# Optimization experiments

Measured on AMD Instinct MI355X. Metric: run time of the kernel, lower is better.

## Reference

```python
import jax, jax.numpy as jnp
import numpy as np

HIDDEN = 128
NUM_TYPES = 13
LN_EPS = 1e-5


def setup_inputs() -> dict:
    key = jax.random.key(0)
    k_adj, k_emb, k_idx, k_w, k_b = jax.random.split(key, 5)
    B, N, M, H, T = 8, 4096, 2048, HIDDEN, NUM_TYPES
    adj = jax.random.uniform(k_adj, (B, N, M), dtype=jnp.float32)
    embeds = jax.random.normal(k_emb, (B, N, H), dtype=jnp.float32)
    node_type_index = jax.random.randint(k_idx, (B, N), 0, T, dtype=jnp.int32)
    node_mask = jnp.ones((B, N), dtype=bool)
    # per-type Linear params (nn.Linear default init ~ U(-1/sqrt(H), 1/sqrt(H)))
    lim = 1.0 / np.sqrt(H)
    W = jax.random.uniform(k_w, (T, H, H), dtype=jnp.float32, minval=-lim, maxval=lim)
    b = jax.random.uniform(k_b, (T, H), dtype=jnp.float32, minval=-lim, maxval=lim)
    gamma = jnp.ones((H,), dtype=jnp.float32)
    beta = jnp.zeros((H,), dtype=jnp.float32)
    return {"adj": adj, "embeds": embeds, "node_type_index": node_type_index,
            "node_mask": node_mask, "W": W, "b": b, "gamma": gamma, "beta": beta}


def reference(adj, embeds, node_type_index, node_mask, W, b, gamma, beta):
    T = W.shape[0]
    # per-node-type linear: compute all T projections, then route by type.
    # y: [T, B, N, H]
    y = jnp.einsum('bnh,thd->tbnd', embeds, W) + b[:, None, None, :]
    onehot = jax.nn.one_hot(node_type_index, T, dtype=embeds.dtype)  # [B, N, T]
    routed = jnp.einsum('tbnd,bnt->bnd', y, onehot)                   # [B, N, H]
    x = jnp.where(node_mask[..., None], routed, embeds)
    # LayerNorm over hidden dim
    mu = jnp.mean(x, axis=-1, keepdims=True)
    var = jnp.mean(jnp.square(x - mu), axis=-1, keepdims=True)
    x = (x - mu) * jax.lax.rsqrt(var + LN_EPS) * gamma + beta
    # two-stage hypergraph aggregation: adj^T @ x, then adj @ lat
    lat = jnp.einsum('bnm,bnh->bmh', adj, x)   # [B, M, H]
    ret = jnp.einsum('bnm,bmh->bnh', adj, lat)  # [B, N, H]
    return ret
```

## Files before the change

### kernel.cpp

```cpp
#include <hip/hip_runtime.h>
#include <stdint.h>
#include <stddef.h>


typedef float    f32x4_t  __attribute__((ext_vector_type(4)));
typedef __bf16   bf16x8_t __attribute__((ext_vector_type(8)));
typedef unsigned int u32x4_t __attribute__((ext_vector_type(4)));
typedef unsigned int u32x2_t __attribute__((ext_vector_type(2)));

__device__ __forceinline__ unsigned short f2bf(float f) {
    union { float f; unsigned int u; } v; v.f = f;
    unsigned int u = v.u;
    return (unsigned short)((u + 0x7FFFu + ((u >> 16) & 1u)) >> 16);
}

__device__ __forceinline__ unsigned int cvtpk(float a, float b) {
    unsigned int r;
    asm("v_cvt_pk_bf16_f32 %0, %1, %2" : "=v"(r) : "v"(a), "v"(b));
    return r;
}

__device__ __forceinline__ bool mask_on(const unsigned char* m, int gid) {
    return (m[gid] | m[(gid >> 2) << 2]) != 0;
}

__device__ __forceinline__ int foff(int row, int g) {
    return row * 128 + (((g) ^ (row & 7)) << 4);
}

template<int GSTRIDE>
__device__ __forceinline__ void stage_B(const unsigned short* __restrict__ gb,
                                        int k0, unsigned short* ldsB, int t)
{
    const int l = t & 63, w = t >> 6;
    const int hsub = l >> 3;
    const int csrc = ((l & 7) ^ hsub) << 3;
    #pragma unroll
    for (int i = 0; i < 4; ++i) {
        const int hbase = i * 32 + w * 8;
        const unsigned short* src = gb + (size_t)(hbase + hsub) * GSTRIDE + k0 + csrc;
        unsigned short* dst = ldsB + hbase * 64;
        __builtin_amdgcn_global_load_lds(
            (__attribute__((address_space(1))) void*)src,
            (__attribute__((address_space(3))) void*)dst, 16, 0, 0);
    }
}

__global__ __launch_bounds__(256) void k0_wtrans(
    const float* __restrict__ W, unsigned short* __restrict__ WT)
{
    __shared__ float tile[128][132];
    const int t = threadIdx.x, ty = blockIdx.x;
    const float* Wt = W + (size_t)ty * 128 * 128;
    for (int it = 0; it < 16; ++it) {
        int idx = it * 256 + t;
        int h = idx >> 5, c = (idx & 31) * 4;
        *(float4*)(&tile[h][c]) = *(const float4*)(Wt + h * 128 + c);
    }
    __syncthreads();
    const int d = t >> 1, half = t & 1, h0 = half * 64;
    unsigned short* out = WT + ((size_t)ty * 128 + d) * 128 + h0;
    #pragma unroll
    for (int ch = 0; ch < 8; ++ch) {
        int h = h0 + ch * 8;
        u32x4_t o;
        o[0] = cvtpk(tile[h + 0][d], tile[h + 1][d]);
        o[1] = cvtpk(tile[h + 2][d], tile[h + 3][d]);
        o[2] = cvtpk(tile[h + 4][d], tile[h + 5][d]);
        o[3] = cvtpk(tile[h + 6][d], tile[h + 7][d]);
        *(u32x4_t*)(out + ch * 8) = o;
    }
}

__global__ __launch_bounds__(256) void k1_typed_ln(
    const float* __restrict__ embeds,
    const int*   __restrict__ ntype,
    const unsigned char* __restrict__ mask8,
    const unsigned short* __restrict__ WT,
    const float* __restrict__ bias,
    const float* __restrict__ gamma,
    const float* __restrict__ beta,
    unsigned short* __restrict__ xT)
{
    __shared__ unsigned short e_lds[64][136];
    __shared__ unsigned short y_lds[64][136];
    __shared__ unsigned short lists[13][64];
    __shared__ int cnt[13];
    __shared__ int grp_ty[32], grp_base[32], grp_n;
    __shared__ unsigned char msk[64];
    __shared__ float g_lds[128], be_lds[128];

    const int t   = threadIdx.x;
    const int bid = blockIdx.x;
    const int b   = bid & 7;
    const int n0  = (bid >> 3) << 6;
    const int gbase = b * 4096 + n0;
    const float* ebase = embeds + (size_t)gbase * 128;

    {
        const int n = t >> 2, q = t & 3;
        const float* src = ebase + n * 128 + q * 32;
        #pragma unroll
        for (int c = 0; c < 4; ++c) {
            f32x4_t va = *(const f32x4_t*)(src + c * 8);
            f32x4_t vb = *(const f32x4_t*)(src + c * 8 + 4);
            u32x4_t o;
            o[0] = cvtpk(va[0], va[1]); o[1] = cvtpk(va[2], va[3]);
            o[2] = cvtpk(vb[0], vb[1]); o[3] = cvtpk(vb[2], vb[3]);
            *(u32x4_t*)(&e_lds[n][q * 32 + c * 8]) = o;
        }
    }
    if (t < 128) { g_lds[t] = gamma[t]; be_lds[t] = beta[t]; }
    if (t < 64)  msk[t] = mask_on(mask8, gbase + t) ? 1 : 0;
    if (t < 13)  cnt[t] = 0;
    __syncthreads();

    if (t < 64) {
        int ty = ntype[(size_t)gbase + t];
        int slot = atomicAdd(&cnt[ty], 1);
        lists[ty][slot] = (unsigned short)t;
    }
    __syncthreads();
    if (t == 0) {
        int g = 0;
        for (int ty = 0; ty < 13; ++ty) {
            int c = cnt[ty];
            for (int base = 0; base < c; base += 16) {
                grp_ty[g] = ty; grp_base[g] = base; ++g;
            }
        }
        grp_n = g;
    }
    __syncthreads();

    const int NG   = grp_n;
    const int lane = t & 63, wv = t >> 6;
    const int fr = lane & 15, fg = lane >> 4;
    const int d0 = wv * 32;

    for (int g = 0; g < NG; ++g) {
        const int ty = grp_ty[g], base = grp_base[g];
        const int cend = cnt[ty] - 1;
        const int nodeA = lists[ty][min(base + fr, cend)];

        bf16x8_t afr[4];
        #pragma unroll
        for (int kk = 0; kk < 4; ++kk)
            afr[kk] = __builtin_bit_cast(bf16x8_t,
                *(const u32x4_t*)(&e_lds[nodeA][kk * 32 + fg * 8]));

        const unsigned short* wt = WT + (size_t)ty * 128 * 128;
        f32x4_t acc0 = f32x4_t{0.f, 0.f, 0.f, 0.f};
        f32x4_t acc1 = f32x4_t{0.f, 0.f, 0.f, 0.f};
        #pragma unroll
        for (int kk = 0; kk < 4; ++kk) {
            bf16x8_t b0 = __builtin_bit_cast(bf16x8_t,
                *(const u32x4_t*)(wt + (size_t)(d0 + fr) * 128 + kk * 32 + fg * 8));
            bf16x8_t b1 = __builtin_bit_cast(bf16x8_t,
                *(const u32x4_t*)(wt + (size_t)(d0 + 16 + fr) * 128 + kk * 32 + fg * 8));
            acc0 = __builtin_amdgcn_mfma_f32_16x16x32_bf16(afr[kk], b0, acc0, 0, 0, 0);
            acc1 = __builtin_amdgcn_mfma_f32_16x16x32_bf16(afr[kk], b1, acc1, 0, 0, 0);
        }

        const float bs0 = bias[ty * 128 + d0 + fr];
        const float bs1 = bias[ty * 128 + d0 + 16 + fr];
        #pragma unroll
        for (int j = 0; j < 4; ++j) {
            const int nd = lists[ty][min(base + fg * 4 + j, cend)];
            if (msk[nd]) {
                y_lds[nd][d0 + fr]      = f2bf(acc0[j] + bs0);
                y_lds[nd][d0 + 16 + fr] = f2bf(acc1[j] + bs1);
            } else {
                y_lds[nd][d0 + fr]      = e_lds[nd][d0 + fr];
                y_lds[nd][d0 + 16 + fr] = e_lds[nd][d0 + 16 + fr];
            }
        }
    }
    __syncthreads();

    for (int i = 0; i < 16; ++i) {
        const int n = wv + i * 4;
        unsigned int u = *(const unsigned int*)(&y_lds[n][lane * 2]);
        float vx = __builtin_bit_cast(float, u << 16);
        float vy = __builtin_bit_cast(float, u & 0xffff0000u);
        float s = vx + vy;
        float q = vx * vx + vy * vy;
        #pragma unroll
        for (int mw = 32; mw >= 1; mw >>= 1) {
            s += __shfl_xor(s, mw);
            q += __shfl_xor(q, mw);
        }
        const float mu  = s * 0.0078125f;
        const float var = q * 0.0078125f - mu * mu;
        const float r   = rsqrtf(var + 1e-5f);
        const float ox = (vx - mu) * r * g_lds[lane * 2]     + be_lds[lane * 2];
        const float oy = (vy - mu) * r * g_lds[lane * 2 + 1] + be_lds[lane * 2 + 1];
        *(unsigned int*)(&y_lds[n][lane * 2]) = cvtpk(ox, oy);
    }
    __syncthreads();

    const int nl = t & 63, hg = t >> 6;
    unsigned short* xrow = xT + (size_t)b * 128 * 4096 + n0 + nl;
    for (int i = 0; i < 32; ++i) {
        const int h = hg * 32 + i;
        xrow[(size_t)h * 4096] = y_lds[nl][h];
    }
}

__global__ __launch_bounds__(256) void k2_lat(
    const float* __restrict__ adj,
    const unsigned short* __restrict__ xT,
    float* __restrict__ pLat)
{
    __shared__ unsigned short Al[2][32 * 64];
    __shared__ unsigned short Bl[2][128 * 64];

    const int t   = threadIdx.x;
    const int bid = blockIdx.x;
    const int b   = bid & 7;
    const int r   = bid >> 3;
    const int m0  = (r & 63) << 5;
    const int nc  = r >> 6;
    const int nbase = nc << 11;
    const float* adjb = adj + (size_t)b * 4096 * 2048;
    const unsigned short* xb = xT + (size_t)b * 128 * 4096;

    const int lane = t & 63, wv = t >> 6;
    const int wm = wv & 1, wh = wv >> 1;

    const int a_kp = t >> 3;
    const int a_m  = (t & 7) << 2;

    const int fr = lane & 15, fg = lane >> 4;
    int offA[2], offB[4][2];
    #pragma unroll
    for (int kk = 0; kk < 2; ++kk) offA[kk] = foff(wm * 16 + fr, kk * 4 + fg);
    #pragma unroll
    for (int j = 0; j < 4; ++j)
        #pragma unroll
        for (int kk = 0; kk < 2; ++kk)
            offB[j][kk] = foff(wh * 64 + j * 16 + fr, kk * 4 + fg);

    f32x4_t ar0, ar1;
    auto LOAD_A = [&](int k0) {
        const float* p = adjb + (size_t)(nbase + k0 + a_kp * 2) * 2048 + m0 + a_m;
        ar0 = *(const f32x4_t*)(p);
        ar1 = *(const f32x4_t*)(p + 2048);
    };
    auto WRITE_A = [&](int buf) {
        const int g = a_kp >> 2, wrd = a_kp & 3;
        #pragma unroll
        for (int j = 0; j < 4; ++j) {
            const int m = a_m + j;
            unsigned int pk = cvtpk(ar0[j], ar1[j]);
            *(unsigned int*)((char*)(&Al[buf][0]) + m * 128 + ((g ^ (m & 7)) << 4) + wrd * 4) = pk;
        }
    };

    f32x4_t acc[4];
    #pragma unroll
    for (int j = 0; j < 4; ++j) acc[j] = f32x4_t{0.f, 0.f, 0.f, 0.f};

    LOAD_A(0);
    stage_B<4096>(xb, nbase, &Bl[0][0], t);
    WRITE_A(0);
    __syncthreads();

    for (int s = 0; s < 32; ++s) {
        const int buf = s & 1;
        if (s < 31) {
            LOAD_A((s + 1) * 64);
            stage_B<4096>(xb, nbase + (s + 1) * 64, &Bl[buf ^ 1][0], t);
        }
        bf16x8_t af[2];
        #pragma unroll
        for (int kk = 0; kk < 2; ++kk)
            af[kk] = __builtin_bit_cast(bf16x8_t,
                *(const u32x4_t*)((const char*)(&Al[buf][0]) + offA[kk]));
        #pragma unroll
        for (int j = 0; j < 4; ++j) {
            #pragma unroll
            for (int kk = 0; kk < 2; ++kk) {
                bf16x8_t bfj = __builtin_bit_cast(bf16x8_t,
                    *(const u32x4_t*)((const char*)(&Bl[buf][0]) + offB[j][kk]));
                acc[j] = __builtin_amdgcn_mfma_f32_16x16x32_bf16(af[kk], bfj, acc[j], 0, 0, 0);
            }
        }
        if (s < 31) WRITE_A(buf ^ 1);
        __syncthreads();
    }

    float* pb = pLat + (size_t)(nc * 8 + b) * 128 * 2048;
    const int mrow = m0 + wm * 16 + (lane >> 4) * 4;
    #pragma unroll
    for (int j = 0; j < 4; ++j) {
        int col = wh * 64 + j * 16 + fr;
        *(f32x4_t*)(pb + (size_t)col * 2048 + mrow) = acc[j];
    }
}

__global__ __launch_bounds__(256) void k2_red(
    const float* __restrict__ pLat,
    unsigned short* __restrict__ latT)
{
    const size_t i4 = ((size_t)blockIdx.x * 256 + threadIdx.x) * 4;
    f32x4_t s = *(const f32x4_t*)(pLat + i4);
    s += *(const f32x4_t*)(pLat + i4 + (size_t)2097152);
    u32x2_t o;
    o[0] = cvtpk(s[0], s[1]);
    o[1] = cvtpk(s[2], s[3]);
    *(u32x2_t*)(latT + i4) = o;
}

__global__ __launch_bounds__(256) void k3_ret(
    const float* __restrict__ adj,
    const unsigned short* __restrict__ latT,
    float* __restrict__ ret)
{
    __shared__ unsigned short Al[2][32 * 64];
    __shared__ unsigned short Bl[2][128 * 64];

    const int t   = threadIdx.x;
    const int bid = blockIdx.x;
    const int b   = bid & 7;
    const int n0  = (bid >> 3) << 5;
    const float* adjb = adj + (size_t)b * 4096 * 2048;
    const unsigned short* lb = latT + (size_t)b * 128 * 2048;

    const int lane = t & 63, wv = t >> 6;
    const int wn = wv & 1, wh = wv >> 1;

    const int a_r = t >> 3;
    const int a_c = t & 7;

    const int fr = lane & 15, fg = lane >> 4;
    int offA[2], offB[4][2];
    #pragma unroll
    for (int kk = 0; kk < 2; ++kk) offA[kk] = foff(wn * 16 + fr, kk * 4 + fg);
    #pragma unroll
    for (int j = 0; j < 4; ++j)
        #pragma unroll
        for (int kk = 0; kk < 2; ++kk)
            offB[j][kk] = foff(wh * 64 + j * 16 + fr, kk * 4 + fg);

    f32x4_t ar0, ar1;
    auto LOAD_A = [&](int k0) {
        const float* p = adjb + (size_t)(n0 + a_r) * 2048 + k0 + a_c * 8;
        ar0 = *(const f32x4_t*)(p);
        ar1 = *(const f32x4_t*)(p + 4);
    };
    auto WRITE_A = [&](int buf) {
        u32x4_t pk;
        pk[0] = cvtpk(ar0[0], ar0[1]);
        pk[1] = cvtpk(ar0[2], ar0[3]);
        pk[2] = cvtpk(ar1[0], ar1[1]);
        pk[3] = cvtpk(ar1[2], ar1[3]);
        *(u32x4_t*)((char*)(&Al[buf][0]) + a_r * 128 + ((a_c ^ (a_r & 7)) << 4)) = pk;
    };

    f32x4_t acc[4];
    #pragma unroll
    for (int j = 0; j < 4; ++j) acc[j] = f32x4_t{0.f, 0.f, 0.f, 0.f};

    LOAD_A(0);
    stage_B<2048>(lb, 0, &Bl[0][0], t);
    WRITE_A(0);
    __syncthreads();

    for (int s = 0; s < 32; ++s) {
        const int buf = s & 1;
        if (s < 31) {
            LOAD_A((s + 1) * 64);
            stage_B<2048>(lb, (s + 1) * 64, &Bl[buf ^ 1][0], t);
        }
        bf16x8_t af[2];
        #pragma unroll
        for (int kk = 0; kk < 2; ++kk)
            af[kk] = __builtin_bit_cast(bf16x8_t,
                *(const u32x4_t*)((const char*)(&Al[buf][0]) + offA[kk]));
        #pragma unroll
        for (int j = 0; j < 4; ++j) {
            #pragma unroll
            for (int kk = 0; kk < 2; ++kk) {
                bf16x8_t bfj = __builtin_bit_cast(bf16x8_t,
                    *(const u32x4_t*)((const char*)(&Bl[buf][0]) + offB[j][kk]));
                acc[j] = __builtin_amdgcn_mfma_f32_16x16x32_bf16(af[kk], bfj, acc[j], 0, 0, 0);
            }
        }
        if (s < 31) WRITE_A(buf ^ 1);
        __syncthreads();
    }

    const int nrow = n0 + wn * 16 + (lane >> 4) * 4;
    #pragma unroll
    for (int j = 0; j < 4; ++j) {
        int col = wh * 64 + j * 16 + fr;
        #pragma unroll
        for (int jj = 0; jj < 4; ++jj) {
            ret[((size_t)b * 4096 + nrow + jj) * 128 + col] = acc[j][jj];
        }
    }
}

extern "C" void kernel_launch(void* const* d_in, const int* in_sizes, int n_in,
                              void* d_out, int out_size, void* d_ws, size_t ws_size,
                              hipStream_t stream) {
    const float* adj    = (const float*)d_in[0];
    const float* embeds = (const float*)d_in[1];
    const int*   ntype  = (const int*)d_in[2];
    const unsigned char* mask8 = (const unsigned char*)d_in[3];
    const float* W      = (const float*)d_in[4];
    const float* bias   = (const float*)d_in[5];
    const float* gamma  = (const float*)d_in[6];
    const float* beta   = (const float*)d_in[7];
    float* ret = (float*)d_out;

    unsigned short* xT   = (unsigned short*)d_ws;
    unsigned short* latT = xT + (size_t)8 * 128 * 4096;
    unsigned short* WT   = latT + (size_t)8 * 128 * 2048;
    float* pLat = (float*)(WT + (size_t)13 * 128 * 128);

    hipLaunchKernelGGL(k0_wtrans, dim3(13), dim3(256), 0, stream, W, WT);
    hipLaunchKernelGGL(k1_typed_ln, dim3(512), dim3(256), 0, stream,
                       embeds, ntype, mask8, WT, bias, gamma, beta, xT);
    hipLaunchKernelGGL(k2_lat, dim3(1024), dim3(256), 0, stream, adj, xT, pLat);
    hipLaunchKernelGGL(k2_red, dim3(2048), dim3(256), 0, stream, pLat, latT);
    hipLaunchKernelGGL(k3_ret, dim3(1024), dim3(256), 0, stream, adj, latT, ret);
}
```

Baseline: 186.5 us.

## Enlarge k2_lat M tile to 128 and split N into four chunks

The adj^T·x kernel now computes a 128-row M tile per block instead of 32, with each wave holding a 4x4 grid of MFMA accumulators. The N reduction is split four ways (1024 each) instead of two, and the reduction kernel sums four partial slabs. The goal is to reuse each staged xT tile across four times more M rows, cutting redundant B loads and raising MFMA density per LDS read. The cost is that the grid drops to 512 blocks, registers and LDS go up (lower occupancy), and pLat holds twice as many partials. The pLat workspace also has to be large enough for four slabs.

```diff
diff --git a/kernel.cpp b/kernel.cpp
--- a/kernel.cpp
+++ b/kernel.cpp
@@ -212,16 +212,16 @@
     const unsigned short* __restrict__ xT,
     float* __restrict__ pLat)
 {
-    __shared__ unsigned short Al[2][32 * 64];
+    __shared__ unsigned short Al[2][128 * 64];
     __shared__ unsigned short Bl[2][128 * 64];
 
     const int t   = threadIdx.x;
     const int bid = blockIdx.x;
     const int b   = bid & 7;
     const int r   = bid >> 3;
-    const int m0  = (r & 63) << 5;
-    const int nc  = r >> 6;
-    const int nbase = nc << 11;
+    const int m0  = (r & 15) << 7;
+    const int nc  = r >> 4;
+    const int nbase = nc << 10;
     const float* adjb = adj + (size_t)b * 4096 * 2048;
     const unsigned short* xb = xT + (size_t)b * 128 * 4096;
 
@@ -229,73 +229,90 @@
     const int wm = wv & 1, wh = wv >> 1;
 
     const int a_kp = t >> 3;
-    const int a_m  = (t & 7) << 2;
+    const int a_mc = t & 7;
 
     const int fr = lane & 15, fg = lane >> 4;
-    int offA[2], offB[4][2];
-    #pragma unroll
-    for (int kk = 0; kk < 2; ++kk) offA[kk] = foff(wm * 16 + fr, kk * 4 + fg);
-    #pragma unroll
-    for (int j = 0; j < 4; ++j)
-        #pragma unroll
-        for (int kk = 0; kk < 2; ++kk)
-            offB[j][kk] = foff(wh * 64 + j * 16 + fr, kk * 4 + fg);
-
-    f32x4_t ar0, ar1;
+    int offA[4][2], offB[4][2];
+    #pragma unroll
+    for (int f = 0; f < 4; ++f)
+        #pragma unroll
+        for (int kk = 0; kk < 2; ++kk) {
+            offA[f][kk] = foff(wm * 64 + f * 16 + fr, kk * 4 + fg);
+            offB[f][kk] = foff(wh * 64 + f * 16 + fr, kk * 4 + fg);
+        }
+
+    f32x4_t ar0[4], ar1[4];
     auto LOAD_A = [&](int k0) {
-        const float* p = adjb + (size_t)(nbase + k0 + a_kp * 2) * 2048 + m0 + a_m;
-        ar0 = *(const f32x4_t*)(p);
-        ar1 = *(const f32x4_t*)(p + 2048);
+        #pragma unroll
+        for (int c = 0; c < 4; ++c) {
+            const float* p = adjb + (size_t)(k0 + 2 * a_kp) * 2048 + m0 + c * 32 + a_mc * 4;
+            ar0[c] = *(const f32x4_t*)(p);
+            ar1[c] = *(const f32x4_t*)(p + 2048);
+        }
     };
+    const int awg = a_kp >> 2, awd = a_kp & 3;
     auto WRITE_A = [&](int buf) {
-        const int g = a_kp >> 2, wrd = a_kp & 3;
-        #pragma unroll
-        for (int j = 0; j < 4; ++j) {
-            const int m = a_m + j;
-            unsigned int pk = cvtpk(ar0[j], ar1[j]);
-            *(unsigned int*)((char*)(&Al[buf][0]) + m * 128 + ((g ^ (m & 7)) << 4) + wrd * 4) = pk;
-        }
+        #pragma unroll
+        for (int c = 0; c < 4; ++c)
+            #pragma unroll
+            for (int j = 0; j < 4; ++j) {
+                const int m = c * 32 + a_mc * 4 + j;
+                *(unsigned int*)((char*)(&Al[buf][0]) + m * 128
+                    + ((awg ^ (m & 7)) << 4) + awd * 4) = cvtpk(ar0[c][j], ar1[c][j]);
+            }
     };
 
-    f32x4_t acc[4];
-    #pragma unroll
-    for (int j = 0; j < 4; ++j) acc[j] = f32x4_t{0.f, 0.f, 0.f, 0.f};
-
-    LOAD_A(0);
+    f32x4_t acc[4][4];
+    #pragma unroll
+    for (int i = 0; i < 4; ++i)
+        #pragma unroll
+        for (int j = 0; j < 4; ++j) acc[i][j] = f32x4_t{0.f, 0.f, 0.f, 0.f};
+
+    LOAD_A(nbase);
     stage_B<4096>(xb, nbase, &Bl[0][0], t);
     WRITE_A(0);
     __syncthreads();
 
-    for (int s = 0; s < 32; ++s) {
+    for (int s = 0; s < 16; ++s) {
         const int buf = s & 1;
-        if (s < 31) {
-            LOAD_A((s + 1) * 64);
+        if (s < 15) {
+            LOAD_A(nbase + (s + 1) * 64);
             stage_B<4096>(xb, nbase + (s + 1) * 64, &Bl[buf ^ 1][0], t);
         }
-        bf16x8_t af[2];
-        #pragma unroll
-        for (int kk = 0; kk < 2; ++kk)
-            af[kk] = __builtin_bit_cast(bf16x8_t,
-                *(const u32x4_t*)((const char*)(&Al[buf][0]) + offA[kk]));
-        #pragma unroll
-        for (int j = 0; j < 4; ++j) {
+        bf16x8_t af[4][2];
+        #pragma unroll
+        for (int mf = 0; mf < 4; ++mf)
             #pragma unroll
-            for (int kk = 0; kk < 2; ++kk) {
-                bf16x8_t bfj = __builtin_bit_cast(bf16x8_t,
-                    *(const u32x4_t*)((const char*)(&Bl[buf][0]) + offB[j][kk]));
-                acc[j] = __builtin_amdgcn_mfma_f32_16x16x32_bf16(af[kk], bfj, acc[j], 0, 0, 0);
-            }
-        }
-        if (s < 31) WRITE_A(buf ^ 1);
+            for (int kk = 0; kk < 2; ++kk)
+                af[mf][kk] = __builtin_bit_cast(bf16x8_t,
+                    *(const u32x4_t*)((const char*)(&Al[buf][0]) + offA[mf][kk]));
+        #pragma unroll
+        for (int hf = 0; hf < 4; ++hf) {
+            bf16x8_t bfr[2];
+            #pragma unroll
+            for (int kk = 0; kk < 2; ++kk)
+                bfr[kk] = __builtin_bit_cast(bf16x8_t,
+                    *(const u32x4_t*)((const char*)(&Bl[buf][0]) + offB[hf][kk]));
+            #pragma unroll
+            for (int mf = 0; mf < 4; ++mf)
+                #pragma unroll
+                for (int kk = 0; kk < 2; ++kk)
+                    acc[mf][hf] = __builtin_amdgcn_mfma_f32_16x16x32_bf16(
+                        af[mf][kk], bfr[kk], acc[mf][hf], 0, 0, 0);
+        }
+        if (s < 15) WRITE_A(buf ^ 1);
         __syncthreads();
     }
 
     float* pb = pLat + (size_t)(nc * 8 + b) * 128 * 2048;
-    const int mrow = m0 + wm * 16 + (lane >> 4) * 4;
-    #pragma unroll
-    for (int j = 0; j < 4; ++j) {
-        int col = wh * 64 + j * 16 + fr;
-        *(f32x4_t*)(pb + (size_t)col * 2048 + mrow) = acc[j];
+    #pragma unroll
+    for (int mf = 0; mf < 4; ++mf) {
+        const int mrow = m0 + wm * 64 + mf * 16 + (lane >> 4) * 4;
+        #pragma unroll
+        for (int hf = 0; hf < 4; ++hf) {
+            const int col = wh * 64 + hf * 16 + fr;
+            *(f32x4_t*)(pb + (size_t)col * 2048 + mrow) = acc[mf][hf];
+        }
     }
 }
 
@@ -305,7 +322,9 @@
 {
     const size_t i4 = ((size_t)blockIdx.x * 256 + threadIdx.x) * 4;
     f32x4_t s = *(const f32x4_t*)(pLat + i4);
-    s += *(const f32x4_t*)(pLat + i4 + (size_t)2097152);
+    #pragma unroll
+    for (int nc = 1; nc < 4; ++nc)
+        s += *(const f32x4_t*)(pLat + i4 + (size_t)nc * 2097152);
     u32x2_t o;
     o[0] = cvtpk(s[0], s[1]);
     o[1] = cvtpk(s[2], s[3]);
@@ -423,7 +442,7 @@
     hipLaunchKernelGGL(k0_wtrans, dim3(13), dim3(256), 0, stream, W, WT);
     hipLaunchKernelGGL(k1_typed_ln, dim3(512), dim3(256), 0, stream,
                        embeds, ntype, mask8, WT, bias, gamma, beta, xT);
-    hipLaunchKernelGGL(k2_lat, dim3(1024), dim3(256), 0, stream, adj, xT, pLat);
+    hipLaunchKernelGGL(k2_lat, dim3(512), dim3(256), 0, stream, adj, xT, pLat);
     hipLaunchKernelGGL(k2_red, dim3(2048), dim3(256), 0, stream, pLat, latT);
     hipLaunchKernelGGL(k3_ret, dim3(1024), dim3(256), 0, stream, adj, latT, ret);
 }
```

Result: faster. 169.4 us (-9.2%).
